# Kernel tuning notes

Measured on AMD Instinct MI355X. Metric: run time of the kernel, lower is better.

The kernel has to match this reference:

```python
import jax, jax.numpy as jnp
import numpy as np

B, L, DIM = 16, 4096, 512
N_FFT, HOP, WIN = 1024, 256, 1024
PAD = (WIN - HOP) // 2  # 'same' padding trim
OUT_DIM = N_FFT + 2


def hann_window(win):
    n = jnp.arange(win, dtype=jnp.float32)
    return 0.5 - 0.5 * jnp.cos(2.0 * jnp.pi * n / win)


def setup_inputs() -> dict:
    key = jax.random.key(0)
    k1, k2 = jax.random.split(key)
    x = jax.random.normal(k1, (B, L, DIM), dtype=jnp.float32)
    W = jax.random.normal(k2, (OUT_DIM, DIM), dtype=jnp.float32) * 0.02
    b = jnp.zeros((OUT_DIM,), dtype=jnp.float32)
    return {"x": x, "W": W, "b": b}


def _istft(S):
    # S: (B, N_FFT//2+1, T) complex rfft spectrum
    T = S.shape[-1]
    frames = jnp.fft.irfft(S, n=N_FFT, axis=1)
    window = hann_window(WIN)
    frames = frames * window[None, :, None]
    out_len = (T - 1) * HOP + WIN
    idx = jnp.arange(T)[:, None] * HOP + jnp.arange(WIN)[None, :]
    fr = frames.transpose(0, 2, 1)
    y = jnp.zeros((fr.shape[0], out_len), fr.dtype).at[:, idx].add(fr)
    env = jnp.zeros((out_len,), fr.dtype).at[idx].add(
        jnp.broadcast_to(window * window, idx.shape))
    y = y[:, PAD:out_len - PAD]
    env = env[PAD:out_len - PAD]
    return y / env


def reference(x, W, b):
    # Linear projection: (B, L, DIM) -> (B, L, N_FFT+2)
    h = jnp.einsum('bld,od->blo', x, W) + b
    h = h.transpose(0, 2, 1)                              # (B, N_FFT+2, L)
    mag, p = jnp.split(h, 2, axis=1)                      # each (B, N_FFT//2+1, L)
    mag = jnp.minimum(jnp.exp(mag), 100.0)                # exp + clip(max=100)
    S = mag * jax.lax.complex(jnp.cos(p), jnp.sin(p))
    return _istft(S)                                      # (B, L*HOP)
```

## Files before the change

### kernel.cpp

```cpp
#include <hip/hip_runtime.h>
#include <hip/hip_bf16.h>
#include <math.h>

#define BATCH   16
#define TFRM    4096
#define DIM     512
#define NFFT    1024
#define HOP     256
#define PADC    384
#define MROWS   (BATCH*TFRM)
#define OUTLEN  1048576
#define TWO_PI_OVER_N 0.006135923151542565f
#define INV_TWO_PI    0.15915494309189535f
#define EPS0    148
#define EPS1    68

typedef __bf16 bf16x8 __attribute__((ext_vector_type(8)));
typedef float  f32x4  __attribute__((ext_vector_type(4)));

__device__ __forceinline__ ushort f2bf(float f) {
  union { float f; unsigned u; } v; v.f = f;
  unsigned u = v.u;
  unsigned r = (u + 0x7FFFu + ((u >> 16) & 1u)) >> 16;
  return (ushort)r;
}
__device__ __forceinline__ float bf2f(ushort h) {
  union { unsigned u; float f; } v; v.u = ((unsigned)h) << 16;
  return v.f;
}
__device__ __forceinline__ float fast_sin(float x) { return __builtin_amdgcn_sinf(x * INV_TWO_PI); }
__device__ __forceinline__ float fast_cos(float x) { return __builtin_amdgcn_cosf(x * INV_TWO_PI); }
__device__ __forceinline__ float fast_exp(float x) { return __builtin_amdgcn_exp2f(x * 1.4426950408889634f); }
__device__ __forceinline__ float dpp_xor1(float v) {
  return __int_as_float(__builtin_amdgcn_update_dpp(
      __float_as_int(v), __float_as_int(v), 0xB1, 0xF, 0xF, false));
}

__global__ void k_prep_x(const float* __restrict__ x, const float* __restrict__ W,
                         const float* __restrict__ bias,
                         ushort* __restrict__ xbf, float* __restrict__ s512) {
  const int row  = blockIdx.x * 4 + (threadIdx.x >> 6);
  const int lane = threadIdx.x & 63;
  const float* xr = x + (size_t)row * DIM + lane * 8;
  float4 v0 = *(const float4*)xr;
  float4 v1 = *(const float4*)(xr + 4);
  ushort4 u0, u1;
  u0.x = f2bf(v0.x); u0.y = f2bf(v0.y); u0.z = f2bf(v0.z); u0.w = f2bf(v0.w);
  u1.x = f2bf(v1.x); u1.y = f2bf(v1.y); u1.z = f2bf(v1.z); u1.w = f2bf(v1.w);
  ushort* xo = xbf + (size_t)row * DIM + lane * 8;
  *(ushort4*)xo = u0;
  *(ushort4*)(xo + 4) = u1;
  const float* w0 = W + 512 * DIM + lane * 8;
  const float* w1 = W + 1025 * DIM + lane * 8;
  float4 a0 = *(const float4*)w0, a1 = *(const float4*)(w0 + 4);
  float4 b0 = *(const float4*)w1, b1 = *(const float4*)(w1 + 4);
  float sm = v0.x*a0.x + v0.y*a0.y + v0.z*a0.z + v0.w*a0.w
           + v1.x*a1.x + v1.y*a1.y + v1.z*a1.z + v1.w*a1.w;
  float sp = v0.x*b0.x + v0.y*b0.y + v0.z*b0.z + v0.w*b0.w
           + v1.x*b1.x + v1.y*b1.y + v1.z*b1.z + v1.w*b1.w;
#pragma unroll
  for (int off = 32; off; off >>= 1) {
    sm += __shfl_down(sm, off);
    sp += __shfl_down(sp, off);
  }
  if (lane == 0) {
    float mag = fminf(fast_exp(sm + bias[512]), 100.0f);
    s512[row] = mag * fast_cos(sp + bias[1025]) * (1.0f / 1024.0f);
  }
}

__global__ void k_prep_w(const float* __restrict__ W, ushort* __restrict__ o) {
  int i = blockIdx.x * 256 + threadIdx.x;
  int j    = i & 7;
  int lane = (i >> 3) & 63;
  int fi   = i >> 9;
  int t    = fi & 15;
  int rg   = fi >> 4;
  int row  = rg * 16 + (lane & 15);
  int col  = t * 32 + ((lane >> 4) << 3) + j;
  int orig = (row >> 1) + (row & 1) * 513;
  o[i] = f2bf(W[orig * DIM + col]);
}

__global__ void k_basis(ushort* __restrict__ basE, ushort* __restrict__ basO) {
  int i = blockIdx.x * 256 + threadIdx.x;
  int j    = i & 7;
  int lane = (i >> 3) & 63;
  int fi   = i >> 9;
  int t    = fi & 15;
  int rg   = fi >> 4;
  int r    = rg * 16 + (lane & 15);
  int k    = t * 32 + ((lane >> 4) << 3) + j;
  int n    = r + 1;
  float e, o;
  if (k == 0) { e = 1.0f / 1024.0f; o = 0.0f; }
  else {
    int ph = (k * n) & 1023;
    float ang = (float)ph * TWO_PI_OVER_N;
    e = 2.0f * cosf(ang) * (1.0f / 1024.0f);
    o = 2.0f * sinf(ang) * (1.0f / 1024.0f);
  }
  basE[i] = f2bf(e);
  basO[i] = f2bf(o);
}

template<int EPI>
__global__ __launch_bounds__(256) void k_gemm(const ushort* A, const ushort* A2, int lda,
                                              const ushort* Bt, const ushort* Bt2,
                                              ushort* C, ushort* C2, int ldc,
                                              int nbn, int NK, int nsplit,
                                              const float* __restrict__ bias,
                                              const float* __restrict__ s512) {
  __shared__ __align__(16) ushort lds[20480];
  const int tid  = threadIdx.x;
  const int cpx  = gridDim.x >> 3;
  int bid  = (blockIdx.x & 7) * cpx + (blockIdx.x >> 3);
  bool second = false;
  if (nsplit > 0 && bid >= nsplit) { second = true; A = A2; Bt = Bt2; C = C2; bid -= nsplit; }
  const int bm   = bid / nbn;
  const int bn   = bid - bm * nbn;
  const int lane = tid & 63;
  const int wv   = tid >> 6;
  const int wr   = (wv >> 1) * 64;
  const int wc   = (wv & 1) * 64;
  const int lr   = lane & 15;
  const int gx   = ((lane >> 4) ^ ((lane >> 1) & 3)) << 3;

  f32x4 acc[4][4] = {};

  const int swz = ((tid & 3) ^ ((tid >> 3) & 3)) << 3;
  const ushort* gA = A + (size_t)(bm * 128 + (tid >> 2)) * lda + swz;
  auto stageA = [&](int t, int slot) {
    const ushort* g0 = gA + t * 32;
    ushort* l = &lds[slot * 4096] + ((tid >> 6) << 9);
    __builtin_amdgcn_global_load_lds(
        (const __attribute__((address_space(1))) void*)g0,
        (__attribute__((address_space(3))) void*)l, 16, 0, 0);
    __builtin_amdgcn_global_load_lds(
        (const __attribute__((address_space(1))) void*)(g0 + (size_t)64 * lda),
        (__attribute__((address_space(3))) void*)(l + 2048), 16, 0, 0);
  };

  const int rg0 = bn * 8 + (wc >> 4);
  const ushort* gBf = Bt + ((size_t)rg0 * 16) * 512 + (size_t)lane * 8;
  auto loadB = [&](int t, bf16x8* bf) {
#pragma unroll
    for (int n = 0; n < 4; ++n) {
      const ushort* p = gBf + (size_t)(n * 16 + t) * 512;
      asm volatile("global_load_dwordx4 %0, %1, off" : "=v"(bf[n]) : "v"(p));
    }
  };

  bf16x8 bE[4], bO[4];

  stageA(0, 0); loadB(0, bE);
  asm volatile("" ::: "memory");
  stageA(1, 1); loadB(1, bO);
  asm volatile("s_waitcnt vmcnt(6)" ::: "memory");
  __builtin_amdgcn_sched_barrier(0);
  __syncthreads();

  int sl = 0;
  for (int t = 0; t < NK; t += 2) {
    const int s0 = sl;
    const int s1 = (s0 >= 2) ? s0 - 2 : s0 + 1;
#pragma unroll
    for (int h = 0; h < 2; ++h) {
      const int u = t + h;
      const int su = h ? s1 : s0;
      const int sp = h ? s0 : ((s0 >= 1) ? s0 - 1 : 2);
      const ushort* lA = &lds[su * 4096];
      bf16x8 aF[4];
#pragma unroll
      for (int m = 0; m < 4; ++m)
        aF[m] = *(const bf16x8*)(lA + (wr + m * 16 + lr) * 32 + gx);
      if (u + 2 < NK) stageA(u + 2, sp);
      if (h == 0) {
#pragma unroll
        for (int m = 0; m < 4; ++m)
#pragma unroll
          for (int n = 0; n < 4; ++n)
            acc[m][n] = __builtin_amdgcn_mfma_f32_16x16x32_bf16(aF[m], bE[n], acc[m][n], 0, 0, 0);
        if (u + 2 < NK) loadB(u + 2, bE);
      } else {
#pragma unroll
        for (int m = 0; m < 4; ++m)
#pragma unroll
          for (int n = 0; n < 4; ++n)
            acc[m][n] = __builtin_amdgcn_mfma_f32_16x16x32_bf16(aF[m], bO[n], acc[m][n], 0, 0, 0);
        if (u + 2 < NK) loadB(u + 2, bO);
      }
      if (u + 2 < NK) {
        asm volatile("s_waitcnt vmcnt(6)" ::: "memory");
        __builtin_amdgcn_sched_barrier(0);
      } else if (u + 1 < NK) {
        asm volatile("s_waitcnt vmcnt(0)" ::: "memory");
        __builtin_amdgcn_sched_barrier(0);
      }
      if (u + 1 < NK) __syncthreads();
    }
    sl = (s1 >= 2) ? s1 - 2 : s1 + 1;
  }

  const int rl = wr + ((lane >> 4) << 2);
  const int r0 = bm * 128 + rl;
  ushort* epi = lds;
  __syncthreads();

  if constexpr (EPI == 0) {
#pragma unroll
    for (int m = 0; m < 4; ++m) {
      float4 sv4 = {0.f, 0.f, 0.f, 0.f};
      if (!second) sv4 = *(const float4*)(s512 + r0 + m * 16);
#pragma unroll
      for (int j = 0; j < 4; ++j) {
        float sv = ((const float*)&sv4)[j];
        int row = rl + m * 16 + j;
#pragma unroll
        for (int n = 0; n < 4; ++n) {
          int c = wc + n * 16 + lr;
          float par = second ? 0.0f : ((c & 1) ? sv : -sv);
          epi[row * EPS0 + c] = f2bf(acc[m][n][j] + par);
        }
      }
    }
    __syncthreads();
#pragma unroll
    for (int i = 0; i < 8; ++i) {
      int row = (tid >> 4) + i * 16;
      int co  = (tid & 15) << 3;
      bf16x8 v = *(const bf16x8*)(epi + row * EPS0 + co);
      *(bf16x8*)(C + (size_t)(bm * 128 + row) * ldc + bn * 128 + co) = v;
    }
  } else {
    ushort* tA = epi;
    ushort* tB = epi + 128 * EPS1;
#pragma unroll
    for (int m = 0; m < 4; ++m) {
#pragma unroll
      for (int n = 0; n < 4; ++n) {
        const int cl  = wc + n * 16 + lr;
        const int kk  = (bn * 128 + cl) >> 1;
        const bool isPhase = (cl & 1);
        const float bs = bias[isPhase ? 513 + kk : kk];
        ushort* dst = (isPhase ? tB : tA);
        const int kkl = cl >> 1;
#pragma unroll
        for (int j = 0; j < 4; ++j) {
          float v = acc[m][n][j] + bs;
          float pv = dpp_xor1(v);
          float hm = isPhase ? pv : v;
          float hp = isPhase ? v : pv;
          float mag = fminf(fast_exp(hm), 100.0f);
          float outv = isPhase ? mag * fast_sin(hp) : mag * fast_cos(hp);
          dst[(rl + m * 16 + j) * EPS1 + kkl] = f2bf(outv);
        }
      }
    }
    __syncthreads();
#pragma unroll
    for (int i = 0; i < 4; ++i) {
      int row = (tid >> 3) + i * 32;
      int co  = (tid & 7) << 3;
      size_t go = (size_t)(bm * 128 + row) * ldc + bn * 64 + co;
      bf16x8 va = *(const bf16x8*)(tA + row * EPS1 + co);
      *(bf16x8*)(C + go) = va;
      bf16x8 vb = *(const bf16x8*)(tB + row * EPS1 + co);
      *(bf16x8*)(C2 + go) = vb;
    }
  }
}

__global__ void k_oa(const ushort* __restrict__ E, const ushort* __restrict__ O,
                     float* __restrict__ out) {
  int u = blockIdx.x * 256 + threadIdx.x;
  int b  = u >> 18;
  int g  = u & 262143;
  int s  = (g << 2) + PADC;
  int t0 = s >> 8;
  int nb = s & 255;
  float acc[4] = {0.f, 0.f, 0.f, 0.f};
  bool interior = (t0 >= 3) && (t0 < TFRM);
  float env[4];
#pragma unroll
  for (int j = 0; j < 4; ++j) env[j] = interior ? 1.5f : 0.0f;
#pragma unroll
  for (int q = 0; q < 4; ++q) {
    int t = t0 - q;
    if (t < 0 || t >= TFRM) continue;
    int n = nb + (q << 8);
    size_t base = ((size_t)(b << 12) + t) << 9;
    float w[4];
#pragma unroll
    for (int j = 0; j < 4; ++j) {
      w[j] = 0.5f - 0.5f * __builtin_amdgcn_cosf((float)(n + j) * (1.0f / 1024.0f));
      if (!interior) env[j] += w[j] * w[j];
    }
    float d[4];
    if (n <= 508) {
      ushort4 e1 = *(const ushort4*)(E + base + n);
      ushort4 o1 = *(const ushort4*)(O + base + n);
      if (n >= 4) {
        ushort4 e0 = *(const ushort4*)(E + base + n - 4);
        ushort4 o0 = *(const ushort4*)(O + base + n - 4);
        d[0] = bf2f(e0.w) - bf2f(o0.w);
      } else d[0] = 0.0f;
      d[1] = bf2f(e1.x) - bf2f(o1.x);
      d[2] = bf2f(e1.y) - bf2f(o1.y);
      d[3] = bf2f(e1.z) - bf2f(o1.z);
    } else if (n == 512) {
      ushort4 e = *(const ushort4*)(E + base + 508);
      ushort4 o = *(const ushort4*)(O + base + 508);
      d[0] = bf2f(e.w) - bf2f(o.w);
      d[1] = bf2f(e.z) + bf2f(o.z);
      d[2] = bf2f(e.y) + bf2f(o.y);
      d[3] = bf2f(e.x) + bf2f(o.x);
    } else {
      ushort4 e = *(const ushort4*)(E + base + 1020 - n);
      ushort4 o = *(const ushort4*)(O + base + 1020 - n);
      d[0] = bf2f(e.w) + bf2f(o.w);
      d[1] = bf2f(e.z) + bf2f(o.z);
      d[2] = bf2f(e.y) + bf2f(o.y);
      d[3] = bf2f(e.x) + bf2f(o.x);
    }
#pragma unroll
    for (int j = 0; j < 4; ++j) acc[j] += w[j] * d[j];
  }
  float4 o4;
  o4.x = acc[0] / env[0]; o4.y = acc[1] / env[1];
  o4.z = acc[2] / env[2]; o4.w = acc[3] / env[3];
  *(float4*)(out + (size_t)u * 4) = o4;
}

extern "C" void kernel_launch(void* const* d_in, const int* in_sizes, int n_in,
                              void* d_out, int out_size, void* d_ws, size_t ws_size,
                              hipStream_t stream) {
  const float* x    = (const float*)d_in[0];
  const float* W    = (const float*)d_in[1];
  const float* bias = (const float*)d_in[2];
  float* out = (float*)d_out;
  char* ws = (char*)d_ws;

  ushort* xbf  = (ushort*)(ws + 0);
  ushort* Epp  = (ushort*)(ws + 0);
  ushort* h_a  = (ushort*)(ws + 67108864);
  ushort* h_b  = (ushort*)(ws + 134217728);
  ushort* Obuf = (ushort*)(ws + 201326592);
  ushort* Wp   = (ushort*)(ws + 268435456);
  ushort* basE = (ushort*)(ws + 269484032);
  ushort* basO = (ushort*)(ws + 270008320);
  float*  s512 = (float*) (ws + 270532608);

  k_prep_x<<<MROWS / 4, 256, 0, stream>>>(x, W, bias, xbf, s512);
  k_prep_w<<<(1024 * 512) / 256, 256, 0, stream>>>(W, Wp);
  k_basis<<<(512 * 512) / 256, 256, 0, stream>>>(basE, basO);

  k_gemm<1><<<(MROWS / 128) * 8, 256, 0, stream>>>(
      xbf, nullptr, DIM, Wp, nullptr, h_a, h_b, 512, 8, 16, 0, bias, nullptr);

  k_gemm<0><<<2 * (MROWS / 128) * 4, 256, 0, stream>>>(
      h_a, h_b, 512, basE, basO, Epp, Obuf, 512, 4, 16, (MROWS / 128) * 4,
      nullptr, s512);

  k_oa<<<(BATCH * OUTLEN) / 1024, 256, 0, stream>>>(Epp, Obuf, out);
}
```

Baseline: 299.5 us.

## Widen GEMM tiles to 128x256 and regroup W rows for lane-local epilogue

Each wave's GEMM tile grows from 64x64 to 64x128 (eight B fragments, 32 accumulators), so the block covers 256 output columns and each staged A tile is reused across twice the columns. The W prep layout changes so magnitude and phase rows sit in alternating 16-row fragments. The first GEMM's epilogue can then pair them within a lane and drop the DPP cross-lane swap. Both epilogues now write through LDS in two half-passes to fit the larger tile. The cost is higher register pressure and possibly lower occupancy, plus half as many blocks in each grid.

```diff
diff --git a/kernel.cpp b/kernel.cpp
--- a/kernel.cpp
+++ b/kernel.cpp
@@ -12,8 +12,6 @@
 #define OUTLEN  1048576
 #define TWO_PI_OVER_N 0.006135923151542565f
 #define INV_TWO_PI    0.15915494309189535f
-#define EPS0    148
-#define EPS1    68
 
 typedef __bf16 bf16x8 __attribute__((ext_vector_type(8)));
 typedef float  f32x4  __attribute__((ext_vector_type(4)));
@@ -31,10 +29,6 @@
 __device__ __forceinline__ float fast_sin(float x) { return __builtin_amdgcn_sinf(x * INV_TWO_PI); }
 __device__ __forceinline__ float fast_cos(float x) { return __builtin_amdgcn_cosf(x * INV_TWO_PI); }
 __device__ __forceinline__ float fast_exp(float x) { return __builtin_amdgcn_exp2f(x * 1.4426950408889634f); }
-__device__ __forceinline__ float dpp_xor1(float v) {
-  return __int_as_float(__builtin_amdgcn_update_dpp(
-      __float_as_int(v), __float_as_int(v), 0xB1, 0xF, 0xF, false));
-}
 
 __global__ void k_prep_x(const float* __restrict__ x, const float* __restrict__ W,
                          const float* __restrict__ bias,
@@ -75,10 +69,10 @@
   int lane = (i >> 3) & 63;
   int fi   = i >> 9;
   int t    = fi & 15;
-  int rg   = fi >> 4;
-  int row  = rg * 16 + (lane & 15);
+  int f    = fi >> 4;
+  int kk   = (f >> 1) * 16 + (lane & 15);
   int col  = t * 32 + ((lane >> 4) << 3) + j;
-  int orig = (row >> 1) + (row & 1) * 513;
+  int orig = (f & 1) ? 513 + kk : kk;
   o[i] = f2bf(W[orig * DIM + col]);
 }
 
@@ -88,8 +82,8 @@
   int lane = (i >> 3) & 63;
   int fi   = i >> 9;
   int t    = fi & 15;
-  int rg   = fi >> 4;
-  int r    = rg * 16 + (lane & 15);
+  int f    = fi >> 4;
+  int r    = f * 16 + (lane & 15);
   int k    = t * 32 + ((lane >> 4) << 3) + j;
   int n    = r + 1;
   float e, o;
@@ -122,11 +116,13 @@
   const int lane = tid & 63;
   const int wv   = tid >> 6;
   const int wr   = (wv >> 1) * 64;
-  const int wc   = (wv & 1) * 64;
+  const int wc   = (wv & 1) * 128;
   const int lr   = lane & 15;
-  const int gx   = ((lane >> 4) ^ ((lane >> 1) & 3)) << 3;
-
-  f32x4 acc[4][4] = {};
+  const int gq   = lane >> 4;
+  const int gq4  = gq << 2;
+  const int gx   = (gq ^ ((lane >> 1) & 3)) << 3;
+
+  f32x4 acc[4][8] = {};
 
   const int swz = ((tid & 3) ^ ((tid >> 3) & 3)) << 3;
   const ushort* gA = A + (size_t)(bm * 128 + (tid >> 2)) * lda + swz;
@@ -141,22 +137,22 @@
         (__attribute__((address_space(3))) void*)(l + 2048), 16, 0, 0);
   };
 
-  const int rg0 = bn * 8 + (wc >> 4);
+  const int rg0 = bn * 16 + (wc >> 4);
   const ushort* gBf = Bt + ((size_t)rg0 * 16) * 512 + (size_t)lane * 8;
   auto loadB = [&](int t, bf16x8* bf) {
 #pragma unroll
-    for (int n = 0; n < 4; ++n) {
+    for (int n = 0; n < 8; ++n) {
       const ushort* p = gBf + (size_t)(n * 16 + t) * 512;
       asm volatile("global_load_dwordx4 %0, %1, off" : "=v"(bf[n]) : "v"(p));
     }
   };
 
-  bf16x8 bE[4], bO[4];
+  bf16x8 bE[8], bO[8];
 
   stageA(0, 0); loadB(0, bE);
   asm volatile("" ::: "memory");
   stageA(1, 1); loadB(1, bO);
-  asm volatile("s_waitcnt vmcnt(6)" ::: "memory");
+  asm volatile("s_waitcnt vmcnt(10)" ::: "memory");
   __builtin_amdgcn_sched_barrier(0);
   __syncthreads();
 
@@ -179,19 +175,19 @@
 #pragma unroll
         for (int m = 0; m < 4; ++m)
 #pragma unroll
-          for (int n = 0; n < 4; ++n)
+          for (int n = 0; n < 8; ++n)
             acc[m][n] = __builtin_amdgcn_mfma_f32_16x16x32_bf16(aF[m], bE[n], acc[m][n], 0, 0, 0);
         if (u + 2 < NK) loadB(u + 2, bE);
       } else {
 #pragma unroll
         for (int m = 0; m < 4; ++m)
 #pragma unroll
-          for (int n = 0; n < 4; ++n)
+          for (int n = 0; n < 8; ++n)
             acc[m][n] = __builtin_amdgcn_mfma_f32_16x16x32_bf16(aF[m], bO[n], acc[m][n], 0, 0, 0);
         if (u + 2 < NK) loadB(u + 2, bO);
       }
       if (u + 2 < NK) {
-        asm volatile("s_waitcnt vmcnt(6)" ::: "memory");
+        asm volatile("s_waitcnt vmcnt(10)" ::: "memory");
         __builtin_amdgcn_sched_barrier(0);
       } else if (u + 1 < NK) {
         asm volatile("s_waitcnt vmcnt(0)" ::: "memory");
@@ -202,71 +198,77 @@
     sl = (s1 >= 2) ? s1 - 2 : s1 + 1;
   }
 
-  const int rl = wr + ((lane >> 4) << 2);
-  const int r0 = bm * 128 + rl;
-  ushort* epi = lds;
   __syncthreads();
 
   if constexpr (EPI == 0) {
-#pragma unroll
-    for (int m = 0; m < 4; ++m) {
-      float4 sv4 = {0.f, 0.f, 0.f, 0.f};
-      if (!second) sv4 = *(const float4*)(s512 + r0 + m * 16);
-#pragma unroll
-      for (int j = 0; j < 4; ++j) {
-        float sv = ((const float*)&sv4)[j];
-        int row = rl + m * 16 + j;
-#pragma unroll
-        for (int n = 0; n < 4; ++n) {
-          int c = wc + n * 16 + lr;
-          float par = second ? 0.0f : ((c & 1) ? sv : -sv);
-          epi[row * EPS0 + c] = f2bf(acc[m][n][j] + par);
+    ushort* epi = lds;
+#pragma unroll
+    for (int p = 0; p < 2; ++p) {
+      if (p) __syncthreads();
+#pragma unroll
+      for (int mm = 0; mm < 2; ++mm) {
+        const int m = 2 * p + mm;
+        const int grow0 = bm * 128 + wr + m * 16 + gq4;
+        float4 sv4 = {0.f, 0.f, 0.f, 0.f};
+        if (!second) sv4 = *(const float4*)(s512 + grow0);
+        const int lr2 = (wr ? 32 : 0) + mm * 16 + gq4;
+#pragma unroll
+        for (int j = 0; j < 4; ++j) {
+          float sv = ((const float*)&sv4)[j];
+#pragma unroll
+          for (int n = 0; n < 8; ++n) {
+            int c = wc + n * 16 + lr;
+            float par = second ? 0.0f : ((c & 1) ? sv : -sv);
+            epi[(lr2 + j) * 260 + c] = f2bf(acc[m][n][j] + par);
+          }
         }
       }
-    }
-    __syncthreads();
-#pragma unroll
-    for (int i = 0; i < 8; ++i) {
-      int row = (tid >> 4) + i * 16;
-      int co  = (tid & 15) << 3;
-      bf16x8 v = *(const bf16x8*)(epi + row * EPS0 + co);
-      *(bf16x8*)(C + (size_t)(bm * 128 + row) * ldc + bn * 128 + co) = v;
+      __syncthreads();
+#pragma unroll
+      for (int it = 0; it < 8; ++it) {
+        int lo = (tid >> 5) + it * 8;
+        int co = (tid & 31) << 3;
+        int grow = bm * 128 + (lo < 32 ? p * 32 + lo : 64 + p * 32 + (lo - 32));
+        bf16x8 v = *(const bf16x8*)(epi + lo * 260 + co);
+        *(bf16x8*)(C + (size_t)grow * ldc + bn * 256 + co) = v;
+      }
     }
   } else {
-    ushort* tA = epi;
-    ushort* tB = epi + 128 * EPS1;
-#pragma unroll
-    for (int m = 0; m < 4; ++m) {
-#pragma unroll
-      for (int n = 0; n < 4; ++n) {
-        const int cl  = wc + n * 16 + lr;
-        const int kk  = (bn * 128 + cl) >> 1;
-        const bool isPhase = (cl & 1);
-        const float bs = bias[isPhase ? 513 + kk : kk];
-        ushort* dst = (isPhase ? tB : tA);
-        const int kkl = cl >> 1;
-#pragma unroll
-        for (int j = 0; j < 4; ++j) {
-          float v = acc[m][n][j] + bs;
-          float pv = dpp_xor1(v);
-          float hm = isPhase ? pv : v;
-          float hp = isPhase ? v : pv;
-          float mag = fminf(fast_exp(hm), 100.0f);
-          float outv = isPhase ? mag * fast_sin(hp) : mag * fast_cos(hp);
-          dst[(rl + m * 16 + j) * EPS1 + kkl] = f2bf(outv);
+    ushort* tA = lds;
+    ushort* tB = lds + 64 * 132;
+#pragma unroll
+    for (int p = 0; p < 2; ++p) {
+      if (p) __syncthreads();
+#pragma unroll
+      for (int mm = 0; mm < 2; ++mm) {
+        const int m = 2 * p + mm;
+        const int lr2 = (wr ? 32 : 0) + mm * 16 + gq4;
+#pragma unroll
+        for (int i = 0; i < 4; ++i) {
+          const int k = (bn * 8 + (wc >> 5) + i) * 16 + lr;
+          const float bmg = bias[k];
+          const float bph = bias[513 + k];
+          const int klocal = ((wc >> 5) + i) * 16 + lr;
+#pragma unroll
+          for (int j = 0; j < 4; ++j) {
+            float hm = acc[m][2 * i][j]     + bmg;
+            float hp = acc[m][2 * i + 1][j] + bph;
+            float mag = fminf(fast_exp(hm), 100.0f);
+            tA[(lr2 + j) * 132 + klocal] = f2bf(mag * fast_cos(hp));
+            tB[(lr2 + j) * 132 + klocal] = f2bf(mag * fast_sin(hp));
+          }
         }
       }
-    }
-    __syncthreads();
-#pragma unroll
-    for (int i = 0; i < 4; ++i) {
-      int row = (tid >> 3) + i * 32;
-      int co  = (tid & 7) << 3;
-      size_t go = (size_t)(bm * 128 + row) * ldc + bn * 64 + co;
-      bf16x8 va = *(const bf16x8*)(tA + row * EPS1 + co);
-      *(bf16x8*)(C + go) = va;
-      bf16x8 vb = *(const bf16x8*)(tB + row * EPS1 + co);
-      *(bf16x8*)(C2 + go) = vb;
+      __syncthreads();
+#pragma unroll
+      for (int it = 0; it < 4; ++it) {
+        int lo = (tid >> 4) + it * 16;
+        int co = (tid & 15) << 3;
+        int grow = bm * 128 + (lo < 32 ? p * 32 + lo : 64 + p * 32 + (lo - 32));
+        size_t go = (size_t)grow * ldc + bn * 128 + co;
+        *(bf16x8*)(C  + go) = *(const bf16x8*)(tA + lo * 132 + co);
+        *(bf16x8*)(C2 + go) = *(const bf16x8*)(tB + lo * 132 + co);
+      }
     }
   }
 }
@@ -355,11 +357,11 @@
   k_prep_w<<<(1024 * 512) / 256, 256, 0, stream>>>(W, Wp);
   k_basis<<<(512 * 512) / 256, 256, 0, stream>>>(basE, basO);
 
-  k_gemm<1><<<(MROWS / 128) * 8, 256, 0, stream>>>(
-      xbf, nullptr, DIM, Wp, nullptr, h_a, h_b, 512, 8, 16, 0, bias, nullptr);
-
-  k_gemm<0><<<2 * (MROWS / 128) * 4, 256, 0, stream>>>(
-      h_a, h_b, 512, basE, basO, Epp, Obuf, 512, 4, 16, (MROWS / 128) * 4,
+  k_gemm<1><<<(MROWS / 128) * 4, 256, 0, stream>>>(
+      xbf, nullptr, DIM, Wp, nullptr, h_a, h_b, 512, 4, 16, 0, bias, nullptr);
+
+  k_gemm<0><<<2 * (MROWS / 128) * 2, 256, 0, stream>>>(
+      h_a, h_b, 512, basE, basO, Epp, Obuf, 512, 2, 16, (MROWS / 128) * 2,
       nullptr, s512);
 
   k_oa<<<(BATCH * OUTLEN) / 1024, 256, 0, stream>>>(Epp, Obuf, out);
```

After: 432.5 us. 44.4% more time.
